# Kernel tuning notes

Measured on AMD Instinct MI355X. Metric: run time of the kernel, lower is better.

## Reference

```python
import jax, jax.numpy as jnp
import numpy as np

N = 100000
H = 20            # horizon
C = 36            # classes
MV = 200000       # vehicle edges
MO = 400000       # obstacle edges
STEP = 2.0        # TRAJECTORY_PIONTS_LENGTH
DIST_COST = 1.0
OBS_COST = 1.0
OBS_RADIUS = 1.0
VEH_COST = 1.0
VEH_RADIUS = 2.0


def setup_inputs() -> dict:
    key = jax.random.key(0)
    k1, k2, k3, k4, k5, k6 = jax.random.split(key, 6)
    # X: [type, x, y, t_x/r, t_y]; all rows vehicles (type 0) so trajectories are live
    feats = jax.random.normal(k1, (N, 4), dtype=jnp.float32) * 10.0
    X = jnp.concatenate([jnp.zeros((N, 1), jnp.float32), feats], axis=1)
    prediction = jax.random.normal(k2, (N, H * C), dtype=jnp.float32)
    ev0 = jax.random.randint(k3, (MV,), 0, N, dtype=jnp.int32)
    off = jax.random.randint(k4, (MV,), 1, N, dtype=jnp.int32)
    ev1 = (ev0 + off) % N  # guarantee no self-edges
    edges_vehicles = jnp.stack([ev0, ev1], axis=0)
    eo0 = jax.random.randint(k5, (MO,), 0, N, dtype=jnp.int32)
    eo1 = jax.random.randint(k6, (MO,), 0, N, dtype=jnp.int32)
    edges_obstacles = jnp.stack([eo0, eo1], axis=0)
    return {"X": X, "prediction": prediction,
            "edges_vehicles": edges_vehicles, "edges_obstacles": edges_obstacles}


def reference(X, prediction, edges_vehicles, edges_obstacles):
    # class decoding: angle = argmax_class * (2pi/C) * max_logit
    pred = prediction.reshape(-1, H, C)
    max_vals = jnp.max(pred, axis=-1)                      # (N,H)
    max_cls = jnp.argmax(pred, axis=-1).astype(pred.dtype)  # (N,H)
    ang = max_cls * (2.0 * np.pi / C) * max_vals
    vec = jnp.stack([jnp.cos(ang), jnp.sin(ang)], axis=-1)  # (N,H,2)

    vmask = X[:, 0] == 0
    # sequential rollout == cumulative sum of unit steps from initial position
    traj = X[:, None, 1:3] + jnp.cumsum(vec * STEP, axis=1)  # (N,H,2)
    traj = jnp.where(vmask[:, None, None], traj, 0.0)

    # distance to target, mean over vehicle rows x horizon
    d = jnp.linalg.norm(X[:, None, 3:5] - traj, axis=-1)    # (N,H)
    nveh = jnp.sum(vmask).astype(d.dtype)
    distance_loss = jnp.sum(jnp.where(vmask[:, None], d, 0.0)) / (nveh * H) * DIST_COST

    # obstacle term: gather obstacle rows and trajectory rows along edges
    fo = X[edges_obstacles[0]]                               # (MO,5)
    tt = traj[edges_obstacles[1]]                            # (MO,H,2)
    od = jnp.linalg.norm(fo[:, None, 1:3] - tt, axis=-1)     # (MO,H)
    onear = od < fo[:, None, 3] + OBS_RADIUS
    osafe = jnp.where(onear, od, 1.0)
    ocnt = jnp.sum(onear)
    osum = jnp.sum(jnp.where(onear, 1.0 / osafe, 0.0))
    obstacle_loss = jnp.where(ocnt > 0, osum / jnp.maximum(ocnt, 1), 0.0) * OBS_COST

    # vehicle term: all-pairs horizon-step distances per edge
    ft = traj[edges_vehicles[0]]                             # (MV,H,2)
    tt2 = traj[edges_vehicles[1]]                            # (MV,H,2)
    vd = jnp.linalg.norm(ft[:, :, None, :] - tt2[:, None, :, :], axis=-1)  # (MV,H,H)
    vnear = vd < VEH_RADIUS
    vsafe = jnp.where(vnear, vd, 1.0)
    vcnt = jnp.sum(vnear)
    vsum = jnp.sum(jnp.where(vnear, 1.0 / vsafe, 0.0))
    vehicle_loss = jnp.where(vcnt > 0, vsum / jnp.maximum(vcnt, 1), 0.0) * VEH_COST

    total = distance_loss + obstacle_loss + vehicle_loss
    return (total, distance_loss, obstacle_loss, vehicle_loss)
```

## Files before the change

kernel.cpp:

```cpp
#include <hip/hip_runtime.h>
#include <math.h>

#define HORIZON 20
#define NCLASS  36
constexpr float STEP = 2.0f;
constexpr float TWO_PI_OVER_C = 0.17453292519943295f;
constexpr float OBS_RADIUS = 1.0f;

template <int BS>
__device__ __forceinline__ void block_commit(float sum, unsigned cnt,
                                             float* __restrict__ pOut,
                                             unsigned* __restrict__ cOut) {
    __shared__ float    ls[BS / 64];
    __shared__ unsigned lc[BS / 64];
    #pragma unroll
    for (int off = 32; off > 0; off >>= 1) {
        sum += __shfl_down(sum, off, 64);
        cnt += __shfl_down(cnt, off, 64);
    }
    int wid = threadIdx.x >> 6;
    if ((threadIdx.x & 63) == 0) { ls[wid] = sum; lc[wid] = cnt; }
    __syncthreads();
    if (threadIdx.x == 0) {
        float s = 0.0f; unsigned c = 0u;
        #pragma unroll
        for (int w = 0; w < BS / 64; w++) { s += ls[w]; c += lc[w]; }
        pOut[blockIdx.x] = s;
        cOut[blockIdx.x] = c;
    }
}

__global__ void __launch_bounds__(256) traj_kernel(const float* __restrict__ X,
                                                   const float* __restrict__ pred,
                                                   float2* __restrict__ traj,
                                                   float* __restrict__ distP,
                                                   unsigned* __restrict__ distC,
                                                   int n) {
    int i = blockIdx.x * 256 + threadIdx.x;
    float dsum = 0.0f;
    unsigned vehc = 0;
    if (i < n) {
        const float* xr = X + (size_t)i * 5;
        float typ = xr[0];
        float px = xr[1], py = xr[2];
        float tx = xr[3], ty = xr[4];
        bool veh = (typ == 0.0f);
        const float4* p = (const float4*)(pred + (size_t)i * (HORIZON * NCLASS));
        float4 outv[10];
        #pragma unroll
        for (int h = 0; h < HORIZON; h++) {
            float4 v[9];
            #pragma unroll
            for (int q = 0; q < 9; q++) v[q] = p[h * 9 + q];
            float best = -INFINITY; int bi = 0;
            #pragma unroll
            for (int q = 0; q < 9; q++) {
                float vals[4] = {v[q].x, v[q].y, v[q].z, v[q].w};
                #pragma unroll
                for (int k = 0; k < 4; k++) {
                    int c = q * 4 + k;
                    if (vals[k] > best) { best = vals[k]; bi = c; }
                }
            }
            float ang = (float)bi * TWO_PI_OVER_C * best;
            float s, c;
            sincosf(ang, &s, &c);
            px += STEP * c; py += STEP * s;
            float ox = veh ? px : 0.0f;
            float oy = veh ? py : 0.0f;
            if (h & 1) { outv[h >> 1].z = ox; outv[h >> 1].w = oy; }
            else       { outv[h >> 1].x = ox; outv[h >> 1].y = oy; }
            float dx = tx - ox, dy = ty - oy;
            dsum += veh ? sqrtf(fmaf(dy, dy, dx * dx)) : 0.0f;
        }
        float4* tp = (float4*)(traj + (size_t)i * HORIZON);
        #pragma unroll
        for (int q = 0; q < 10; q++) tp[q] = outv[q];
        vehc = veh ? 1u : 0u;
    }
    block_commit<256>(dsum, vehc, distP, distC);
}

__global__ void __launch_bounds__(256) obstacle_kernel(const float* __restrict__ X,
                                                       const int* __restrict__ eo,
                                                       const float2* __restrict__ traj,
                                                       float* __restrict__ obsP,
                                                       unsigned* __restrict__ obsC,
                                                       int mo) {
    int e = blockIdx.x * 256 + threadIdx.x;
    float osum = 0.0f; unsigned ocnt = 0;
    if (e < mo) {
        int src = eo[e];
        int dst = eo[mo + e];
        const float* xr = X + (size_t)src * 5;
        float fx = xr[1], fy = xr[2];
        float thr = xr[3] + OBS_RADIUS;
        float thr2 = thr * thr;
        bool tpos = thr > 0.0f;
        const float4* tp = (const float4*)(traj + (size_t)dst * HORIZON);
        float4 buf[10];
        #pragma unroll
        for (int q = 0; q < 10; q++) buf[q] = tp[q];
        const float* f = (const float*)buf;
        #pragma unroll
        for (int h = 0; h < HORIZON; h++) {
            float dx = fx - f[2 * h], dy = fy - f[2 * h + 1];
            float d2 = fmaf(dy, dy, dx * dx);
            bool near = tpos && (d2 < thr2);
            ocnt += near ? 1u : 0u;
            osum += near ? rsqrtf(d2) : 0.0f;
        }
    }
    block_commit<256>(osum, ocnt, obsP, obsC);
}

__global__ void __launch_bounds__(256) vehicle_kernel(const int* __restrict__ ev,
                                                      const float2* __restrict__ traj,
                                                      float* __restrict__ vehP,
                                                      unsigned* __restrict__ vehC,
                                                      int mv) {
    int t = blockIdx.x * 256 + threadIdx.x;
    int e = t >> 1;
    int half = t & 1;
    float vsum = 0.0f; unsigned vcnt = 0;
    if (e < mv) {
        int a = ev[e];
        int b = ev[mv + e];
        const float4* pb = (const float4*)(traj + (size_t)b * HORIZON);
        float4 tb[10];
        #pragma unroll
        for (int q = 0; q < 10; q++) tb[q] = pb[q];
        const float* fb = (const float*)tb;
        const float2* pa = traj + (size_t)a * HORIZON + half * 10;
        for (int i = 0; i < 10; i++) {
            float2 av = pa[i];
            #pragma unroll
            for (int j = 0; j < HORIZON; j++) {
                float dx = av.x - fb[2 * j];
                float dy = av.y - fb[2 * j + 1];
                float d2 = fmaf(dy, dy, dx * dx);
                bool near = d2 < 4.0f;
                vcnt += near ? 1u : 0u;
                vsum += near ? rsqrtf(d2) : 0.0f;
            }
        }
    }
    block_commit<256>(vsum, vcnt, vehP, vehC);
}

__global__ void __launch_bounds__(256) finalize_kernel(
        const float* __restrict__ distP, const unsigned* __restrict__ distC, int nbR,
        const float* __restrict__ obsP,  const unsigned* __restrict__ obsC,  int nbO,
        const float* __restrict__ vehP,  const unsigned* __restrict__ vehC,  int nbV,
        float* __restrict__ out) {
    double s0 = 0, s1 = 0, s2 = 0;
    unsigned long long c0 = 0, c1 = 0, c2 = 0;
    for (int i = threadIdx.x; i < nbR; i += 256) { s0 += (double)distP[i]; c0 += distC[i]; }
    for (int i = threadIdx.x; i < nbO; i += 256) { s1 += (double)obsP[i];  c1 += obsC[i]; }
    for (int i = threadIdx.x; i < nbV; i += 256) { s2 += (double)vehP[i];  c2 += vehC[i]; }
    __shared__ double ds[3][4];
    __shared__ unsigned long long dc[3][4];
    double sv[3] = {s0, s1, s2};
    unsigned long long cv[3] = {c0, c1, c2};
    #pragma unroll
    for (int k = 0; k < 3; k++) {
        double v = sv[k]; unsigned long long cc = cv[k];
        #pragma unroll
        for (int off = 32; off > 0; off >>= 1) {
            v += __shfl_down(v, off, 64);
            cc += __shfl_down(cc, off, 64);
        }
        if ((threadIdx.x & 63) == 0) { ds[k][threadIdx.x >> 6] = v; dc[k][threadIdx.x >> 6] = cc; }
    }
    __syncthreads();
    if (threadIdx.x == 0) {
        double S[3]; unsigned long long C[3];
        #pragma unroll
        for (int k = 0; k < 3; k++) {
            S[k] = ds[k][0] + ds[k][1] + ds[k][2] + ds[k][3];
            C[k] = dc[k][0] + dc[k][1] + dc[k][2] + dc[k][3];
        }
        float dist = (C[0] > 0) ? (float)(S[0] / ((double)C[0] * (double)HORIZON)) : 0.0f;
        float obs  = (C[1] > 0) ? (float)(S[1] / (double)C[1]) : 0.0f;
        float veh  = (C[2] > 0) ? (float)(S[2] / (double)C[2]) : 0.0f;
        out[0] = dist + obs + veh;
        out[1] = dist;
        out[2] = obs;
        out[3] = veh;
    }
}

extern "C" void kernel_launch(void* const* d_in, const int* in_sizes, int n_in,
                              void* d_out, int out_size, void* d_ws, size_t ws_size,
                              hipStream_t stream) {
    const float* X    = (const float*)d_in[0];
    const float* pred = (const float*)d_in[1];
    const int*   ev   = (const int*)d_in[2];
    const int*   eo   = (const int*)d_in[3];
    int n_nodes = in_sizes[0] / 5;
    int mv = in_sizes[2] / 2;
    int mo = in_sizes[3] / 2;

    int nbR = (n_nodes + 255) / 256;
    int nbO = (mo + 255) / 256;
    int nbV = (2 * mv + 255) / 256;

    char* w = (char*)d_ws;
    float2* traj = (float2*)w;
    size_t off = (size_t)n_nodes * HORIZON * sizeof(float2);
    off = (off + 255) & ~(size_t)255;
    float*    distP = (float*)(w + off);    off += (size_t)nbR * 4;
    unsigned* distC = (unsigned*)(w + off); off += (size_t)nbR * 4;
    float*    obsP  = (float*)(w + off);    off += (size_t)nbO * 4;
    unsigned* obsC  = (unsigned*)(w + off); off += (size_t)nbO * 4;
    float*    vehP  = (float*)(w + off);    off += (size_t)nbV * 4;
    unsigned* vehC  = (unsigned*)(w + off); off += (size_t)nbV * 4;
    float* out = (float*)d_out;

    hipLaunchKernelGGL(traj_kernel, dim3(nbR), dim3(256), 0, stream,
                       X, pred, traj, distP, distC, n_nodes);
    hipLaunchKernelGGL(obstacle_kernel, dim3(nbO), dim3(256), 0, stream,
                       X, eo, traj, obsP, obsC, mo);
    hipLaunchKernelGGL(vehicle_kernel, dim3(nbV), dim3(256), 0, stream,
                       ev, traj, vehP, vehC, mv);
    hipLaunchKernelGGL(finalize_kernel, dim3(1), dim3(256), 0, stream,
                       distP, distC, nbR, obsP, obsC, nbO, vehP, vehC, nbV, out);
}
```

Before: 487.1 us.

## Split trajectory kernel into coalesced argmax/angle pass and rollout pass

The fused trajectory kernel had each thread read its own 2880-byte prediction row with strided float4 loads, which coalesce poorly. A new angles kernel has each wave read contiguous float4s, take a per-float4 max in registers, and finish the 36-class argmax per horizon row through shared memory before writing a step vector. A separate rollout kernel then does the cumulative sum and distance term from the step buffer. This costs an extra launch and an extra round trip of the step buffer through global memory.

Result: faster. 474.6 us (-2.6%).

```diff
diff --git a/kernel.cpp b/kernel.cpp
--- a/kernel.cpp
+++ b/kernel.cpp
@@ -30,12 +30,52 @@
     }
 }
 
-__global__ void __launch_bounds__(256) traj_kernel(const float* __restrict__ X,
-                                                   const float* __restrict__ pred,
-                                                   float2* __restrict__ traj,
-                                                   float* __restrict__ distP,
-                                                   unsigned* __restrict__ distC,
-                                                   int n) {
+__global__ void __launch_bounds__(256) angles_kernel(const float* __restrict__ pred,
+                                                     float2* __restrict__ steps,
+                                                     int total_rows) {
+    __shared__ float2 sm[4][576];
+    int wave = threadIdx.x >> 6;
+    int lane = threadIdx.x & 63;
+    int chunk = blockIdx.x * 4 + wave;
+    int row0 = chunk * 64;
+    int total_f4 = total_rows * 9;
+    const float4* p4 = (const float4*)pred;
+    #pragma unroll
+    for (int q = 0; q < 9; q++) {
+        int gl = q * 64 + lane;
+        int g = row0 * 9 + gl;
+        float4 v;
+        if (g < total_f4) v = p4[g];
+        else v = make_float4(-INFINITY, -INFINITY, -INFINITY, -INFINITY);
+        int j = gl % 9;
+        float m = v.x; int ii = 0;
+        if (v.y > m) { m = v.y; ii = 1; }
+        if (v.z > m) { m = v.z; ii = 2; }
+        if (v.w > m) { m = v.w; ii = 3; }
+        sm[wave][gl] = make_float2(m, (float)(j * 4 + ii));
+    }
+    __syncthreads();
+    int row = row0 + lane;
+    if (row < total_rows) {
+        float best = -INFINITY; float bidx = 0.0f;
+        #pragma unroll
+        for (int j = 0; j < 9; j++) {
+            float2 e = sm[wave][lane * 9 + j];
+            if (e.x > best) { best = e.x; bidx = e.y; }
+        }
+        float ang = bidx * TWO_PI_OVER_C * best;
+        float s, c;
+        sincosf(ang, &s, &c);
+        steps[row] = make_float2(STEP * c, STEP * s);
+    }
+}
+
+__global__ void __launch_bounds__(256) rollout_kernel(const float* __restrict__ X,
+                                                      const float2* __restrict__ steps,
+                                                      float2* __restrict__ traj,
+                                                      float* __restrict__ distP,
+                                                      unsigned* __restrict__ distC,
+                                                      int n) {
     int i = blockIdx.x * 256 + threadIdx.x;
     float dsum = 0.0f;
     unsigned vehc = 0;
@@ -45,37 +85,23 @@
         float px = xr[1], py = xr[2];
         float tx = xr[3], ty = xr[4];
         bool veh = (typ == 0.0f);
-        const float4* p = (const float4*)(pred + (size_t)i * (HORIZON * NCLASS));
-        float4 outv[10];
+        const float4* sp = (const float4*)(steps + (size_t)i * HORIZON);
+        float4 buf[10];
+        #pragma unroll
+        for (int q = 0; q < 10; q++) buf[q] = sp[q];
+        float* f = (float*)buf;
         #pragma unroll
         for (int h = 0; h < HORIZON; h++) {
-            float4 v[9];
-            #pragma unroll
-            for (int q = 0; q < 9; q++) v[q] = p[h * 9 + q];
-            float best = -INFINITY; int bi = 0;
-            #pragma unroll
-            for (int q = 0; q < 9; q++) {
-                float vals[4] = {v[q].x, v[q].y, v[q].z, v[q].w};
-                #pragma unroll
-                for (int k = 0; k < 4; k++) {
-                    int c = q * 4 + k;
-                    if (vals[k] > best) { best = vals[k]; bi = c; }
-                }
-            }
-            float ang = (float)bi * TWO_PI_OVER_C * best;
-            float s, c;
-            sincosf(ang, &s, &c);
-            px += STEP * c; py += STEP * s;
+            px += f[2 * h]; py += f[2 * h + 1];
             float ox = veh ? px : 0.0f;
             float oy = veh ? py : 0.0f;
-            if (h & 1) { outv[h >> 1].z = ox; outv[h >> 1].w = oy; }
-            else       { outv[h >> 1].x = ox; outv[h >> 1].y = oy; }
+            f[2 * h] = ox; f[2 * h + 1] = oy;
             float dx = tx - ox, dy = ty - oy;
             dsum += veh ? sqrtf(fmaf(dy, dy, dx * dx)) : 0.0f;
         }
         float4* tp = (float4*)(traj + (size_t)i * HORIZON);
         #pragma unroll
-        for (int q = 0; q < 10; q++) tp[q] = outv[q];
+        for (int q = 0; q < 10; q++) tp[q] = buf[q];
         vehc = veh ? 1u : 0u;
     }
     block_commit<256>(dsum, vehc, distP, distC);
@@ -201,13 +227,19 @@
     int mv = in_sizes[2] / 2;
     int mo = in_sizes[3] / 2;
 
+    int total_rows = n_nodes * HORIZON;
+    int nChunks = (total_rows + 63) / 64;
+    int nbA = (nChunks + 3) / 4;
     int nbR = (n_nodes + 255) / 256;
     int nbO = (mo + 255) / 256;
     int nbV = (2 * mv + 255) / 256;
 
     char* w = (char*)d_ws;
-    float2* traj = (float2*)w;
-    size_t off = (size_t)n_nodes * HORIZON * sizeof(float2);
+    float2* steps = (float2*)w;
+    size_t off = (size_t)total_rows * sizeof(float2);
+    off = (off + 255) & ~(size_t)255;
+    float2* traj = (float2*)(w + off);
+    off += (size_t)total_rows * sizeof(float2);
     off = (off + 255) & ~(size_t)255;
     float*    distP = (float*)(w + off);    off += (size_t)nbR * 4;
     unsigned* distC = (unsigned*)(w + off); off += (size_t)nbR * 4;
@@ -217,8 +249,10 @@
     unsigned* vehC  = (unsigned*)(w + off); off += (size_t)nbV * 4;
     float* out = (float*)d_out;
 
-    hipLaunchKernelGGL(traj_kernel, dim3(nbR), dim3(256), 0, stream,
-                       X, pred, traj, distP, distC, n_nodes);
+    hipLaunchKernelGGL(angles_kernel, dim3(nbA), dim3(256), 0, stream,
+                       pred, steps, total_rows);
+    hipLaunchKernelGGL(rollout_kernel, dim3(nbR), dim3(256), 0, stream,
+                       X, steps, traj, distP, distC, n_nodes);
     hipLaunchKernelGGL(obstacle_kernel, dim3(nbO), dim3(256), 0, stream,
                        X, eo, traj, obsP, obsC, mo);
     hipLaunchKernelGGL(vehicle_kernel, dim3(nbV), dim3(256), 0, stream,
```
